# Kernel tuning notes

Hardware: AMD Instinct MI355X
Metric: run time of the kernel (lower is better)

The kernel has to match this reference:

```python
import jax, jax.numpy as jnp
import numpy as np
import math

B, N, D = 2, 4096, 1024
NUM_LAYERS = 12
INIT_RANGE = 0.02


def setup_inputs() -> dict:
    key = jax.random.key(0)
    k1, k2 = jax.random.split(key)
    hidden_states = jax.random.normal(k1, (B, N, D), dtype=jnp.float32)
    std = INIT_RANGE / math.sqrt(2.0 * NUM_LAYERS * D)
    queries = jax.random.normal(k2, (D, D), dtype=jnp.float32) * std
    return {"hidden_states": hidden_states, "queries": queries}


def reference(hidden_states, queries):
    # Q = F.linear(X, W) = X @ W^T  -> [B, N, D]
    q = jnp.einsum('bnd,ed->bne', hidden_states, queries)
    # pre_attn = Q @ X^T  -> [B, N, N]
    pre_attn = jnp.einsum('bne,bme->bnm', q, hidden_states)
    # attention = pre_attn @ X  -> [B, N, D]
    attention = jnp.einsum('bnm,bmd->bnd', pre_attn, hidden_states)
    return attention
```

## Files before the change

### kernel.cpp

```cpp
#include <hip/hip_runtime.h>
#include <hip/hip_bf16.h>
#include <stdint.h>

using bf16 = __hip_bfloat16;
typedef __attribute__((ext_vector_type(8))) short short8;
typedef __attribute__((ext_vector_type(4))) float f32x4;

#define BM 128
#define BK 32

__device__ __forceinline__ void g2lds16(const void* g, void* l) {
    __builtin_amdgcn_global_load_lds(
        (const __attribute__((address_space(1))) void*)g,
        (__attribute__((address_space(3))) void*)l,
        16, 0, 0);
}

__device__ __forceinline__ short f2bs(float x) {
    union { bf16 h; short s; } u;
    u.h = __float2bfloat16(x);
    return u.s;
}

__device__ __forceinline__ int bswz(int row, int cg) { return cg ^ ((row >> 1) & 3); }
__device__ __forceinline__ int fswz(int row, int cg) { return cg ^ (row & 7); }

__global__ __launch_bounds__(256)
void transpose_cvt(const float* __restrict__ src, ushort* __restrict__ dstT,
                   ushort* __restrict__ dstN,
                   int R, int C, long sstride, long dstrideT, long dstrideN)
{
    __shared__ __align__(16) ushort t[64][72];
    const float* s = src + (size_t)blockIdx.z * sstride;
    ushort*      dT = dstT + (size_t)blockIdx.z * dstrideT;
    const int r0 = blockIdx.y * 64, c0 = blockIdx.x * 64;
    const int tid = threadIdx.x;
#pragma unroll
    for (int ii = 0; ii < 4; ++ii) {
        int idx = ii * 256 + tid;
        int r = idx >> 4, c4 = (idx & 15) * 4;
        float4 v = *(const float4*)&s[(size_t)(r0 + r) * C + c0 + c4];
        union { ushort u[4]; uint2 q; } o;
        o.u[0] = (ushort)f2bs(v.x); o.u[1] = (ushort)f2bs(v.y);
        o.u[2] = (ushort)f2bs(v.z); o.u[3] = (ushort)f2bs(v.w);
        *(uint2*)&t[r][c4] = o.q;
        if (dstN) {
            ushort* dN = dstN + (size_t)blockIdx.z * dstrideN;
            *(uint2*)&dN[(size_t)(r0 + r) * C + c0 + c4] = o.q;
        }
    }
    __syncthreads();
#pragma unroll
    for (int ii = 0; ii < 2; ++ii) {
        int idx = ii * 256 + tid;
        int c = idx >> 3, r8 = (idx & 7) * 8;
        union { ushort u[8]; uint4 v; } tmp;
#pragma unroll
        for (int j = 0; j < 8; ++j) tmp.u[j] = t[r8 + j][c];
        *(uint4*)&dT[(size_t)(c0 + c) * R + r0 + r8] = tmp.v;
    }
}

template <int MODE, int A_F32, int NFRAG>
__global__ __launch_bounds__(256)
void gemm_bt(const void* __restrict__ Av, const bf16* __restrict__ B,
             void* __restrict__ Cv, int M, int N, int K, int kChunks,
             long sA, long sB, long sC)
{
    constexpr int BN  = 32 * NFRAG;
    constexpr int BSH = BN / 64;
    __shared__ __align__(16) bf16 lA[2][BM * BK * (A_F32 ? 2 : 1)];
    __shared__ __align__(16) bf16 lB[2][BN * BK];

    const int z     = blockIdx.z;
    const int batch = z / kChunks;
    const int chunk = z - batch * kChunks;
    const int kLen  = K / kChunks;
    const int k0    = chunk * kLen;

    const int m0 = blockIdx.y * BM;
    const int n0 = blockIdx.x * BN;

    const int tid  = threadIdx.x;
    const int lane = tid & 63;
    const int wave = tid >> 6;
    const int wr   = wave >> 1, wc = wave & 1;
    const int ml   = lane & 15;
    const int q    = lane >> 4;

    const bf16* Bb = B + (size_t)batch * sB;
    const bf16* bp[BSH];
#pragma unroll
    for (int s = 0; s < BSH; ++s) {
        int idx = s * 256 + tid;
        int row = idx >> 2, cg = idx & 3;
        bp[s] = Bb + (size_t)(n0 + row) * K + k0 + 8 * bswz(row, cg);
    }

    const float* a32[4];
    const bf16*  a16[2];
    if constexpr (A_F32) {
        const float* Ab = (const float*)Av + (size_t)batch * sA;
#pragma unroll
        for (int s = 0; s < 4; ++s) {
            int idx = s * 256 + tid;
            int row = idx >> 3, cg = idx & 7;
            a32[s] = Ab + (size_t)(m0 + row) * K + k0 + 4 * fswz(row, cg);
        }
    } else {
        const bf16* Ab = (const bf16*)Av + (size_t)batch * sA;
#pragma unroll
        for (int s = 0; s < 2; ++s) {
            int idx = s * 256 + tid;
            int row = idx >> 2, cg = idx & 3;
            a16[s] = Ab + (size_t)(m0 + row) * K + k0 + 8 * bswz(row, cg);
        }
    }

    auto stage = [&](int buf) {
        if constexpr (A_F32) {
            float* lAf = (float*)lA[buf];
#pragma unroll
            for (int s = 0; s < 4; ++s) {
                g2lds16(a32[s], &lAf[(s * 256 + tid) * 4]);
                a32[s] += BK;
            }
        } else {
#pragma unroll
            for (int s = 0; s < 2; ++s) {
                g2lds16(a16[s], &lA[buf][(s * 256 + tid) * 8]);
                a16[s] += BK;
            }
        }
#pragma unroll
        for (int s = 0; s < BSH; ++s) {
            g2lds16(bp[s], &lB[buf][(s * 256 + tid) * 8]);
            bp[s] += BK;
        }
    };

    f32x4 acc[4][NFRAG] = {};

    const int nk = kLen / BK;
    stage(0);
    for (int kt = 0; kt < nk; ++kt) {
        const int cur = kt & 1;
        __syncthreads();
        if (kt + 1 < nk) stage(cur ^ 1);

        short8 af[4], bfr[NFRAG];
#pragma unroll
        for (int i = 0; i < 4; ++i) {
            const int rA = wr * 64 + i * 16 + ml;
            if constexpr (A_F32) {
                const float* lAf = (const float*)lA[cur];
                float4 x0 = *(const float4*)&lAf[rA * 32 + 4 * fswz(rA, 2 * q)];
                float4 x1 = *(const float4*)&lAf[rA * 32 + 4 * fswz(rA, 2 * q + 1)];
                af[i][0] = f2bs(x0.x); af[i][1] = f2bs(x0.y);
                af[i][2] = f2bs(x0.z); af[i][3] = f2bs(x0.w);
                af[i][4] = f2bs(x1.x); af[i][5] = f2bs(x1.y);
                af[i][6] = f2bs(x1.z); af[i][7] = f2bs(x1.w);
            } else {
                af[i] = *(const short8*)&lA[cur][rA * 32 + 8 * bswz(rA, q)];
            }
        }
#pragma unroll
        for (int j = 0; j < NFRAG; ++j) {
            const int rB = wc * (16 * NFRAG) + j * 16 + ml;
            bfr[j] = *(const short8*)&lB[cur][rB * 32 + 8 * bswz(rB, q)];
        }
#pragma unroll
        for (int mi = 0; mi < 4; ++mi)
#pragma unroll
            for (int nj = 0; nj < NFRAG; ++nj)
                acc[mi][nj] = __builtin_amdgcn_mfma_f32_16x16x32_bf16(
                    af[mi], bfr[nj], acc[mi][nj], 0, 0, 0);
    }

#pragma unroll
    for (int mi = 0; mi < 4; ++mi)
#pragma unroll
        for (int nj = 0; nj < NFRAG; ++nj)
#pragma unroll
            for (int r = 0; r < 4; ++r) {
                int row = m0 + wr * 64 + mi * 16 + q * 4 + r;
                int col = n0 + wc * (16 * NFRAG) + nj * 16 + ml;
                if constexpr (MODE == 1) {
                    float* Cf = (float*)Cv + (size_t)batch * sC;
                    atomicAdd(&Cf[(size_t)row * N + col], acc[mi][nj][r]);
                } else if constexpr (MODE == 0) {
                    ushort* Cb = (ushort*)Cv + (size_t)batch * sC;
                    Cb[(size_t)row * N + col] = (ushort)f2bs(acc[mi][nj][r]);
                } else {
                    float* Cf = (float*)Cv + (size_t)batch * sC;
                    Cf[(size_t)row * N + col] = acc[mi][nj][r];
                }
            }
}

extern "C" void kernel_launch(void* const* d_in, const int* in_sizes, int n_in,
                              void* d_out, int out_size, void* d_ws, size_t ws_size,
                              hipStream_t stream)
{
    const int B = 2, N = 4096, D = 1024;
    const float* X = (const float*)d_in[0];
    const float* W = (const float*)d_in[1];
    float* out = (float*)d_out;

    char* ob = (char*)d_out;
    char* ws = (char*)d_ws;
    ushort* Xt = (ushort*)ob;
    float*  Gf = (float*)(ob + (16ll << 20));
    ushort* Wt = (ushort*)(ob + (28ll << 20));

    const bool bigws = ws_size >= (20ull << 20);
    ushort* Xb = bigws ? (ushort*)ws : nullptr;
    ushort* Mt = (ushort*)(ws + (bigws ? (16ll << 20) : 0));

    transpose_cvt<<<dim3(D / 64, N / 64, B), 256, 0, stream>>>(
        X, Xt, Xb, N, D, (long)N * D, (long)D * N, (long)N * D);
    transpose_cvt<<<dim3(D / 64, D / 64, 1), 256, 0, stream>>>(
        W, Wt, nullptr, D, D, 0, 0, 0);
    (void)hipMemsetAsync(Gf, 0, (size_t)B * D * D * sizeof(float), stream);
    gemm_bt<1, 0, 2><<<dim3(D / 64, D / BM, B * 4), 256, 0, stream>>>(
        (const void*)Xt, (const bf16*)Xt, Gf, D, D, N, 4,
        (long)D * N, (long)D * N, (long)D * D);
    gemm_bt<0, 1, 2><<<dim3(D / 64, D / BM, B), 256, 0, stream>>>(
        (const void*)Gf, (const bf16*)Wt, Mt, D, D, D, 1,
        (long)D * D, 0, (long)D * D);
    if (bigws) {
        gemm_bt<2, 0, 2><<<dim3(D / 64, N / BM, B), 256, 0, stream>>>(
            (const void*)Xb, (const bf16*)Mt, out, N, D, D, 1,
            (long)N * D, (long)D * D, (long)N * D);
    } else {
        gemm_bt<2, 1, 2><<<dim3(D / 64, N / BM, B), 256, 0, stream>>>(
            (const void*)X, (const bf16*)Mt, out, N, D, D, 1,
            (long)N * D, (long)D * D, (long)N * D);
    }
}
```

Baseline: 198.6 us.

## Replace LDS-staged block GEMM with single-wave register-direct GEMM tiles

```diff
diff --git a/kernel.cpp b/kernel.cpp
--- a/kernel.cpp
+++ b/kernel.cpp
@@ -6,24 +6,11 @@
 typedef __attribute__((ext_vector_type(8))) short short8;
 typedef __attribute__((ext_vector_type(4))) float f32x4;
 
-#define BM 128
-#define BK 32
-
-__device__ __forceinline__ void g2lds16(const void* g, void* l) {
-    __builtin_amdgcn_global_load_lds(
-        (const __attribute__((address_space(1))) void*)g,
-        (__attribute__((address_space(3))) void*)l,
-        16, 0, 0);
-}
-
 __device__ __forceinline__ short f2bs(float x) {
     union { bf16 h; short s; } u;
     u.h = __float2bfloat16(x);
     return u.s;
 }
-
-__device__ __forceinline__ int bswz(int row, int cg) { return cg ^ ((row >> 1) & 3); }
-__device__ __forceinline__ int fswz(int row, int cg) { return cg ^ (row & 7); }
 
 __global__ __launch_bounds__(256)
 void transpose_cvt(const float* __restrict__ src, ushort* __restrict__ dstT,
@@ -61,116 +48,71 @@
     }
 }
 
-template <int MODE, int A_F32, int NFRAG>
-__global__ __launch_bounds__(256)
-void gemm_bt(const void* __restrict__ Av, const bf16* __restrict__ B,
+template <int MODE, int A_F32, int MFRAG, int NFRAG>
+__global__ __launch_bounds__(64, 4)
+void gemm_wv(const void* __restrict__ Av, const bf16* __restrict__ B,
              void* __restrict__ Cv, int M, int N, int K, int kChunks,
              long sA, long sB, long sC)
 {
-    constexpr int BN  = 32 * NFRAG;
-    constexpr int BSH = BN / 64;
-    __shared__ __align__(16) bf16 lA[2][BM * BK * (A_F32 ? 2 : 1)];
-    __shared__ __align__(16) bf16 lB[2][BN * BK];
-
     const int z     = blockIdx.z;
     const int batch = z / kChunks;
     const int chunk = z - batch * kChunks;
     const int kLen  = K / kChunks;
     const int k0    = chunk * kLen;
-
-    const int m0 = blockIdx.y * BM;
-    const int n0 = blockIdx.x * BN;
-
-    const int tid  = threadIdx.x;
-    const int lane = tid & 63;
-    const int wave = tid >> 6;
-    const int wr   = wave >> 1, wc = wave & 1;
-    const int ml   = lane & 15;
-    const int q    = lane >> 4;
+    const int m0    = blockIdx.y * (MFRAG * 16);
+    const int n0    = blockIdx.x * (NFRAG * 16);
+    const int lane  = threadIdx.x;
+    const int ml    = lane & 15;
+    const int q     = lane >> 4;
 
     const bf16* Bb = B + (size_t)batch * sB;
-    const bf16* bp[BSH];
+    const bf16* bp[NFRAG];
 #pragma unroll
-    for (int s = 0; s < BSH; ++s) {
-        int idx = s * 256 + tid;
-        int row = idx >> 2, cg = idx & 3;
-        bp[s] = Bb + (size_t)(n0 + row) * K + k0 + 8 * bswz(row, cg);
-    }
+    for (int f = 0; f < NFRAG; ++f)
+        bp[f] = Bb + (size_t)(n0 + f * 16 + ml) * K + k0 + q * 8;
 
-    const float* a32[4];
-    const bf16*  a16[2];
+    const float* af32[MFRAG];
+    const bf16*  af16[MFRAG];
     if constexpr (A_F32) {
         const float* Ab = (const float*)Av + (size_t)batch * sA;
 #pragma unroll
-        for (int s = 0; s < 4; ++s) {
-            int idx = s * 256 + tid;
-            int row = idx >> 3, cg = idx & 7;
-            a32[s] = Ab + (size_t)(m0 + row) * K + k0 + 4 * fswz(row, cg);
-        }
+        for (int f = 0; f < MFRAG; ++f)
+            af32[f] = Ab + (size_t)(m0 + f * 16 + ml) * K + k0 + q * 8;
     } else {
         const bf16* Ab = (const bf16*)Av + (size_t)batch * sA;
 #pragma unroll
-        for (int s = 0; s < 2; ++s) {
-            int idx = s * 256 + tid;
-            int row = idx >> 2, cg = idx & 3;
-            a16[s] = Ab + (size_t)(m0 + row) * K + k0 + 8 * bswz(row, cg);
-        }
+        for (int f = 0; f < MFRAG; ++f)
+            af16[f] = Ab + (size_t)(m0 + f * 16 + ml) * K + k0 + q * 8;
     }
 
-    auto stage = [&](int buf) {
-        if constexpr (A_F32) {
-            float* lAf = (float*)lA[buf];
+    f32x4 acc[MFRAG][NFRAG] = {};
+
+    const int nk = kLen / 32;
+#pragma unroll 4
+    for (int kt = 0; kt < nk; ++kt) {
+        short8 af[MFRAG], bfr[NFRAG];
 #pragma unroll
-            for (int s = 0; s < 4; ++s) {
-                g2lds16(a32[s], &lAf[(s * 256 + tid) * 4]);
-                a32[s] += BK;
-            }
-        } else {
+        for (int f = 0; f < NFRAG; ++f) {
+            bfr[f] = *(const short8*)bp[f];
+            bp[f] += 32;
+        }
 #pragma unroll
-            for (int s = 0; s < 2; ++s) {
-                g2lds16(a16[s], &lA[buf][(s * 256 + tid) * 8]);
-                a16[s] += BK;
+        for (int f = 0; f < MFRAG; ++f) {
+            if constexpr (A_F32) {
+                float4 x0 = *(const float4*)af32[f];
+                float4 x1 = *(const float4*)(af32[f] + 4);
+                af32[f] += 32;
+                af[f][0] = f2bs(x0.x); af[f][1] = f2bs(x0.y);
+                af[f][2] = f2bs(x0.z); af[f][3] = f2bs(x0.w);
+                af[f][4] = f2bs(x1.x); af[f][5] = f2bs(x1.y);
+                af[f][6] = f2bs(x1.z); af[f][7] = f2bs(x1.w);
+            } else {
+                af[f] = *(const short8*)af16[f];
+                af16[f] += 32;
             }
         }
 #pragma unroll
-        for (int s = 0; s < BSH; ++s) {
-            g2lds16(bp[s], &lB[buf][(s * 256 + tid) * 8]);
-            bp[s] += BK;
-        }
-    };
-
-    f32x4 acc[4][NFRAG] = {};
-
-    const int nk = kLen / BK;
-    stage(0);
-    for (int kt = 0; kt < nk; ++kt) {
-        const int cur = kt & 1;
-        __syncthreads();
-        if (kt + 1 < nk) stage(cur ^ 1);
-
-        short8 af[4], bfr[NFRAG];
-#pragma unroll
-        for (int i = 0; i < 4; ++i) {
-            const int rA = wr * 64 + i * 16 + ml;
-            if constexpr (A_F32) {
-                const float* lAf = (const float*)lA[cur];
-                float4 x0 = *(const float4*)&lAf[rA * 32 + 4 * fswz(rA, 2 * q)];
-                float4 x1 = *(const float4*)&lAf[rA * 32 + 4 * fswz(rA, 2 * q + 1)];
-                af[i][0] = f2bs(x0.x); af[i][1] = f2bs(x0.y);
-                af[i][2] = f2bs(x0.z); af[i][3] = f2bs(x0.w);
-                af[i][4] = f2bs(x1.x); af[i][5] = f2bs(x1.y);
-                af[i][6] = f2bs(x1.z); af[i][7] = f2bs(x1.w);
-            } else {
-                af[i] = *(const short8*)&lA[cur][rA * 32 + 8 * bswz(rA, q)];
-            }
-        }
-#pragma unroll
-        for (int j = 0; j < NFRAG; ++j) {
-            const int rB = wc * (16 * NFRAG) + j * 16 + ml;
-            bfr[j] = *(const short8*)&lB[cur][rB * 32 + 8 * bswz(rB, q)];
-        }
-#pragma unroll
-        for (int mi = 0; mi < 4; ++mi)
+        for (int mi = 0; mi < MFRAG; ++mi)
 #pragma unroll
             for (int nj = 0; nj < NFRAG; ++nj)
                 acc[mi][nj] = __builtin_amdgcn_mfma_f32_16x16x32_bf16(
@@ -178,13 +120,13 @@
     }
 
 #pragma unroll
-    for (int mi = 0; mi < 4; ++mi)
+    for (int mi = 0; mi < MFRAG; ++mi)
 #pragma unroll
         for (int nj = 0; nj < NFRAG; ++nj)
 #pragma unroll
             for (int r = 0; r < 4; ++r) {
-                int row = m0 + wr * 64 + mi * 16 + q * 4 + r;
-                int col = n0 + wc * (16 * NFRAG) + nj * 16 + ml;
+                int row = m0 + mi * 16 + q * 4 + r;
+                int col = n0 + nj * 16 + ml;
                 if constexpr (MODE == 1) {
                     float* Cf = (float*)Cv + (size_t)batch * sC;
                     atomicAdd(&Cf[(size_t)row * N + col], acc[mi][nj][r]);
@@ -222,18 +164,18 @@
     transpose_cvt<<<dim3(D / 64, D / 64, 1), 256, 0, stream>>>(
         W, Wt, nullptr, D, D, 0, 0, 0);
     (void)hipMemsetAsync(Gf, 0, (size_t)B * D * D * sizeof(float), stream);
-    gemm_bt<1, 0, 2><<<dim3(D / 64, D / BM, B * 4), 256, 0, stream>>>(
+    gemm_wv<1, 0, 4, 2><<<dim3(D / 32, D / 64, B * 4), 64, 0, stream>>>(
         (const void*)Xt, (const bf16*)Xt, Gf, D, D, N, 4,
         (long)D * N, (long)D * N, (long)D * D);
-    gemm_bt<0, 1, 2><<<dim3(D / 64, D / BM, B), 256, 0, stream>>>(
+    gemm_wv<0, 1, 4, 2><<<dim3(D / 32, D / 64, B), 64, 0, stream>>>(
         (const void*)Gf, (const bf16*)Wt, Mt, D, D, D, 1,
         (long)D * D, 0, (long)D * D);
     if (bigws) {
-        gemm_bt<2, 0, 2><<<dim3(D / 64, N / BM, B), 256, 0, stream>>>(
+        gemm_wv<2, 0, 4, 2><<<dim3(D / 32, N / 64, B), 64, 0, stream>>>(
             (const void*)Xb, (const bf16*)Mt, out, N, D, D, 1,
             (long)N * D, (long)D * D, (long)N * D);
     } else {
-        gemm_bt<2, 1, 2><<<dim3(D / 64, N / BM, B), 256, 0, stream>>>(
+        gemm_wv<2, 1, 4, 2><<<dim3(D / 32, N / 64, B), 64, 0, stream>>>(
             (const void*)X, (const bf16*)Mt, out, N, D, D, 1,
             (long)N * D, (long)D * D, (long)N * D);
     }
```

New measurement: 358.1 us. 80.3% more time.
